# Kernel optimization log

Hardware: AMD Instinct MI355X
Metric: run time of the kernel (lower is better)

## Reference

```python
import jax, jax.numpy as jnp
import numpy as np

N_NODES = 50000
N_EDGES = 800000
D_IN = 128
D_HID = 128
GN_EPS = 1e-5
L2_EPS = 1e-12


def _gcn_conv(x, edge_index, W, b, num_nodes):
    """PyG GCNConv: symmetric normalization with self-loops; x [N, Fin]."""
    src, dst = edge_index[0], edge_index[1]
    loops = jnp.arange(num_nodes, dtype=src.dtype)
    src = jnp.concatenate([src, loops])
    dst = jnp.concatenate([dst, loops])
    ew = jnp.ones(src.shape[0], dtype=x.dtype)
    deg = jax.ops.segment_sum(ew, dst, num_segments=num_nodes)
    dinv = jnp.where(deg > 0, jax.lax.rsqrt(deg), 0.0)
    norm = dinv[src] * dinv[dst]                       # [E+N]
    xw = x @ W                                         # [N, Fout]
    msg = xw[src] * norm[:, None]                      # gather + scale
    out = jax.ops.segment_sum(msg, dst, num_segments=num_nodes)
    return out + b


def _message_norm(x, msg, scale):
    """PyG MessageNorm(learn_scale=True): x + scale * ||x|| * msg/||msg||."""
    msg_n = msg / jnp.maximum(jnp.linalg.norm(msg, axis=-1, keepdims=True), L2_EPS)
    x_norm = jnp.linalg.norm(x, axis=-1, keepdims=True)
    return x + scale * x_norm * msg_n


def _graph_norm(x, weight, bias, mean_scale):
    """PyG GraphNorm, single graph (batch all zeros)."""
    mean = jnp.mean(x, axis=0, keepdims=True)
    out = x - mean * mean_scale
    var = jnp.mean(out * out, axis=0, keepdims=True)
    return weight * out * jax.lax.rsqrt(var + GN_EPS) + bias


def _gelu(x):
    return jax.nn.gelu(x, approximate=False)


def setup_inputs() -> dict:
    key = jax.random.key(0)
    ks = jax.random.split(key, 4)
    X = jax.random.normal(ks[0], (D_IN, N_NODES), dtype=jnp.float32)
    edge_index = jax.random.randint(ks[1], (2, N_EDGES), 0, N_NODES, dtype=jnp.int64)
    W1 = jax.random.normal(ks[2], (D_IN, D_HID), dtype=jnp.float32) * (1.0 / np.sqrt(D_IN))
    b1 = jnp.zeros((D_HID,), dtype=jnp.float32)
    scale1 = jnp.ones((1,), dtype=jnp.float32)
    W2 = jax.random.normal(ks[3], (D_HID, D_IN), dtype=jnp.float32) * (1.0 / np.sqrt(D_HID))
    b2 = jnp.zeros((D_IN,), dtype=jnp.float32)
    scale2 = jnp.ones((1,), dtype=jnp.float32)
    gn_weight = jnp.ones((D_IN,), dtype=jnp.float32)
    gn_bias = jnp.zeros((D_IN,), dtype=jnp.float32)
    gn_mean_scale = jnp.ones((D_IN,), dtype=jnp.float32)
    return {"X": X, "edge_index": edge_index, "W1": W1, "b1": b1, "scale1": scale1,
            "W2": W2, "b2": b2, "scale2": scale2, "gn_weight": gn_weight,
            "gn_bias": gn_bias, "gn_mean_scale": gn_mean_scale}


def reference(X, edge_index, W1, b1, scale1, W2, b2, scale2,
              gn_weight, gn_bias, gn_mean_scale):
    x = X.T                                            # [N, D_IN]
    n = x.shape[0]
    # GCNChain 1
    f = _gelu(_message_norm(x, _gcn_conv(x, edge_index, W1, b1, n), scale1))
    # GCNChain 2
    f = _gelu(_message_norm(f, _gcn_conv(f, edge_index, W2, b2, n), scale2))
    # residual + GraphNorm + GELU
    return _gelu(_graph_norm(f + x, gn_weight, gn_bias, gn_mean_scale))
```

## Files before the change

kernel.cpp:

```cpp
#include <hip/hip_runtime.h>
#include <math.h>

#define D 128
#define CAP 64
#define NBUCK 98
#define BSZ   512
#define CAPB  10240

typedef _Float16 h8 __attribute__((ext_vector_type(8)));
typedef float f4x __attribute__((ext_vector_type(4)));

__device__ __forceinline__ float gelu_f(float v){
    return 0.5f * v * (1.0f + erff(v * 0.70710678f));
}

__global__ void k_init(float* colsum, float* colsq, int* gcur,
                       const float* __restrict__ W1, const float* __restrict__ W2,
                       _Float16* __restrict__ wz1, _Float16* __restrict__ wz2){
    int i = blockIdx.x*blockDim.x + threadIdx.x;
    if (i < D){ colsum[i] = 0.f; colsq[i] = 0.f; }
    if (i < NBUCK) gcur[i] = 0;
    if (i < 32768){
        const float* W = (i < 16384) ? W1 : W2;
        _Float16* wz   = (i < 16384) ? wz1 : wz2;
        int u = i & 16383;
        int jj = u & 7, l = (u>>3)&63, fi = u>>9;
        int kb = fi>>3, j = fi&7;
        int k = kb*32 + (l>>4)*8 + jj;
        int c = j*16 + (l&15);
        wz[u] = (_Float16)W[k*D + c];
    }
}

__global__ __launch_bounds__(256)
void k_part(const int* __restrict__ ei, int* __restrict__ gcur,
            unsigned int* __restrict__ ebin, int E){
    __shared__ int bcnt[NBUCK], bbase[NBUCK], bcur[NBUCK];
    int t = threadIdx.x;
    int chunk = (E + gridDim.x - 1) / gridDim.x;
    int e0 = blockIdx.x*chunk, e1 = min(e0 + chunk, E);
    if (t < NBUCK){ bcnt[t] = 0; bcur[t] = 0; }
    __syncthreads();
    int sl[13], dl[13];
    #pragma unroll
    for (int k = 0; k < 13; k++){
        int e = e0 + t + k*256;
        sl[k] = -1;
        if (e < e1){
            sl[k] = __builtin_nontemporal_load(&ei[e]);
            dl[k] = __builtin_nontemporal_load(&ei[E + e]);
            atomicAdd(&bcnt[dl[k] >> 9], 1);
        }
    }
    __syncthreads();
    if (t < NBUCK) bbase[t] = atomicAdd(&gcur[t], bcnt[t]);
    __syncthreads();
    #pragma unroll
    for (int k = 0; k < 13; k++){
        if (sl[k] >= 0){
            int d = dl[k], b = d >> 9;
            int p = atomicAdd(&bcur[b], 1);
            int idx = bbase[b] + p;
            if (idx < CAPB)
                ebin[(size_t)b*CAPB + idx] = ((unsigned)(d & (BSZ-1)) << 16) | (unsigned)sl[k];
        }
    }
}

__global__ __launch_bounds__(256)
void k_fill2(const unsigned int* __restrict__ ebin, const int* __restrict__ gcur,
             int* __restrict__ cnt, unsigned short* __restrict__ csrc, int N){
    __shared__ unsigned short slab[BSZ*CAP];
    __shared__ int lcnt[BSZ];
    int b = blockIdx.x, t = threadIdx.x;
    for (int i = t; i < BSZ; i += 256) lcnt[i] = 0;
    __syncthreads();
    int cntb = gcur[b]; if (cntb > CAPB) cntb = CAPB;
    const unsigned int* bp = ebin + (size_t)b*CAPB;
    for (int e = t; e < cntb; e += 256){
        unsigned pk = __builtin_nontemporal_load(&bp[e]);
        int dl = pk >> 16;
        int p = atomicAdd(&lcnt[dl], 1);
        if (p < CAP) slab[dl*CAP + p] = (unsigned short)(pk & 0xFFFF);
    }
    __syncthreads();
    int base = b*BSZ;
    int nvalid = N - base; if (nvalid > BSZ) nvalid = BSZ; if (nvalid < 0) nvalid = 0;
    uint4* dst = (uint4*)&csrc[(size_t)base*CAP];
    const uint4* src = (const uint4*)slab;
    for (int i = t; i < nvalid*8; i += 256) dst[i] = src[i];
    for (int i = t; i < nvalid; i += 256) cnt[base + i] = lcnt[i];
}

__launch_bounds__(256)
__global__ void k_gemm_mfma(const float* __restrict__ in, const h8* __restrict__ wz,
                            const int* __restrict__ cnt, _Float16* __restrict__ outh,
                            h8* __restrict__ xt16, int N){
    __shared__ _Float16 a_lds[8192];
    int t = threadIdx.x;
    int n0 = blockIdx.x * 64;

    #pragma unroll
    for (int i = 0; i < 32; i++){
        int idx = i*256 + t;
        int k = idx >> 6, nn = idx & 63;
        int n = n0 + nn;
        float v = (n < N) ? in[(size_t)k*N + n] : 0.f;
        int kb = k>>5, ks = k&31;
        int lane = (ks>>3)*16 + (nn&15);
        int w = nn>>4;
        a_lds[((kb*4 + w)*64 + lane)*8 + (ks&7)] = (_Float16)v;
    }
    __syncthreads();

    int w = t>>6, l = t&63;
    f4x acc[8];
    #pragma unroll
    for (int j = 0; j < 8; j++) acc[j] = (f4x){0.f, 0.f, 0.f, 0.f};
    #pragma unroll
    for (int kb = 0; kb < 4; kb++){
        h8 a = *(const h8*)&a_lds[((kb*4 + w)*64 + l)*8];
        #pragma unroll
        for (int j = 0; j < 8; j++){
            h8 b = wz[(kb*8 + j)*64 + l];
            acc[j] = __builtin_amdgcn_mfma_f32_16x16x32_f16(a, b, acc[j], 0, 0, 0);
        }
    }

    int quad = l>>4, m = l&15;
    #pragma unroll
    for (int r = 0; r < 4; r++){
        int node = n0 + w*16 + quad*4 + r;
        if (node < N){
            float dv = rsqrtf((float)(cnt[node] + 1));
            #pragma unroll
            for (int j = 0; j < 8; j++)
                outh[(size_t)node*D + j*16 + m] = (_Float16)(acc[j][r] * dv);
        }
    }

    {
        int node = t>>2, kb = t&3;
        int n = n0 + node;
        if (n < N){
            #pragma unroll
            for (int q = 0; q < 4; q++){
                h8 v = *(const h8*)&a_lds[((kb*4 + (node>>4))*64 + q*16 + (node&15))*8];
                xt16[(size_t)n*16 + kb*4 + q] = v;
            }
        }
    }
}

__launch_bounds__(256)
__global__ void k_gath1(const h8* __restrict__ y, const h8* __restrict__ resid,
                        const int* __restrict__ cnt,
                        const unsigned short* __restrict__ csrc,
                        const float* __restrict__ bias, const float* __restrict__ scale,
                        const h8* __restrict__ wz,
                        h8* __restrict__ f1out, _Float16* __restrict__ y2out, int N){
    __shared__ _Float16 a_lds[16*17*8];
    int t = threadIdx.x;
    int n0 = blockIdx.x * 16;
    int g = t >> 4, lane = t & 15;
    int n = n0 + g;
    bool valid = (n < N);

    h8 a0 = {0,0,0,0,0,0,0,0}, a1 = a0, a2 = a0, a3 = a0;
    int m = 0; float dv = 1.f;
    if (valid){
        int mraw = cnt[n];
        dv = rsqrtf((float)(mraw + 1));
        m = (mraw < CAP) ? mraw : CAP;
        a0 = y[(size_t)n*16 + lane];
    }
    const unsigned short* sp = csrc + (size_t)n*CAP;
    int j = 0;
    for (; j + 8 <= m; j += 8){
        int s0 = sp[j+0], s1 = sp[j+1], s2 = sp[j+2], s3 = sp[j+3];
        int s4 = sp[j+4], s5 = sp[j+5], s6 = sp[j+6], s7 = sp[j+7];
        h8 v0 = y[(size_t)s0*16 + lane];
        h8 v1 = y[(size_t)s1*16 + lane];
        h8 v2 = y[(size_t)s2*16 + lane];
        h8 v3 = y[(size_t)s3*16 + lane];
        h8 v4 = y[(size_t)s4*16 + lane];
        h8 v5 = y[(size_t)s5*16 + lane];
        h8 v6 = y[(size_t)s6*16 + lane];
        h8 v7 = y[(size_t)s7*16 + lane];
        a0 += v0; a1 += v1; a2 += v2; a3 += v3;
        a0 += v4; a1 += v5; a2 += v6; a3 += v7;
    }
    for (; j + 4 <= m; j += 4){
        int s0 = sp[j+0], s1 = sp[j+1], s2 = sp[j+2], s3 = sp[j+3];
        h8 v0 = y[(size_t)s0*16 + lane];
        h8 v1 = y[(size_t)s1*16 + lane];
        h8 v2 = y[(size_t)s2*16 + lane];
        h8 v3 = y[(size_t)s3*16 + lane];
        a0 += v0; a1 += v1; a2 += v2; a3 += v3;
    }
    for (; j < m; j++) a1 += y[(size_t)sp[j]*16 + lane];
    h8 ah = (a0 + a1) + (a2 + a3);

    const float4* bp = (const float4*)&bias[lane*8];
    float4 b0 = bp[0], b1v = bp[1];
    float c[8], r[8];
    float nc = 0.f, nr = 0.f;
    h8 rv = {0,0,0,0,0,0,0,0};
    if (valid) rv = resid[(size_t)n*16 + lane];
    #pragma unroll
    for (int i = 0; i < 8; i++){
        float bb = (i < 4) ? (&b0.x)[i] : (&b1v.x)[i-4];
        c[i] = bb + dv * (float)ah[i];
        nc += c[i]*c[i];
        r[i] = (float)rv[i];
        nr += r[i]*r[i];
    }
    #pragma unroll
    for (int mm = 8; mm > 0; mm >>= 1){
        nc += __shfl_xor(nc, mm, 64);
        nr += __shfl_xor(nr, mm, 64);
    }
    float scl = scale[0] * sqrtf(nr) / fmaxf(sqrtf(nc), 1e-12f);
    h8 o = {0,0,0,0,0,0,0,0};
    if (valid){
        #pragma unroll
        for (int i = 0; i < 8; i++) o[i] = (_Float16)gelu_f(r[i] + scl*c[i]);
        f1out[(size_t)n*16 + lane] = o;
    }
    *(h8*)&a_lds[(g*17 + lane)*8] = o;
    __syncthreads();

    int w = t >> 6, l = t & 63;
    f4x acc0 = {0.f,0.f,0.f,0.f}, acc1 = acc0;
    #pragma unroll
    for (int kb = 0; kb < 4; kb++){
        h8 a = *(const h8*)&a_lds[((l&15)*17 + kb*4 + (l>>4))*8];
        h8 bb0 = wz[(kb*8 + w*2+0)*64 + l];
        h8 bb1 = wz[(kb*8 + w*2+1)*64 + l];
        acc0 = __builtin_amdgcn_mfma_f32_16x16x32_f16(a, bb0, acc0, 0, 0, 0);
        acc1 = __builtin_amdgcn_mfma_f32_16x16x32_f16(a, bb1, acc1, 0, 0, 0);
    }
    int quad = l >> 4, mc = l & 15;
    #pragma unroll
    for (int r2 = 0; r2 < 4; r2++){
        int node = n0 + quad*4 + r2;
        if (node < N){
            float dvn = rsqrtf((float)(cnt[node] + 1));
            y2out[(size_t)node*D + (w*2+0)*16 + mc] = (_Float16)(acc0[r2] * dvn);
            y2out[(size_t)node*D + (w*2+1)*16 + mc] = (_Float16)(acc1[r2] * dvn);
        }
    }
}

__launch_bounds__(256)
__global__ void k_gather2(const h8* __restrict__ y, const h8* __restrict__ resid,
                          const h8* __restrict__ xorig,
                          const int* __restrict__ cnt,
                          const unsigned short* __restrict__ csrc,
                          const float* __restrict__ bias, const float* __restrict__ scale,
                          h8* __restrict__ out16, int N){
    int n = blockIdx.x*16 + (threadIdx.x >> 4);
    if (n >= N) return;
    int lane = threadIdx.x & 15;
    h8 a0 = y[(size_t)n*16 + lane];
    h8 a1 = {0,0,0,0,0,0,0,0}, a2 = a1, a3 = a1;
    int mraw = cnt[n];
    float dv = rsqrtf((float)(mraw + 1));
    int m = (mraw < CAP) ? mraw : CAP;
    const unsigned short* sp = csrc + (size_t)n*CAP;
    int j = 0;
    for (; j + 8 <= m; j += 8){
        int s0 = sp[j+0], s1 = sp[j+1], s2 = sp[j+2], s3 = sp[j+3];
        int s4 = sp[j+4], s5 = sp[j+5], s6 = sp[j+6], s7 = sp[j+7];
        h8 v0 = y[(size_t)s0*16 + lane];
        h8 v1 = y[(size_t)s1*16 + lane];
        h8 v2 = y[(size_t)s2*16 + lane];
        h8 v3 = y[(size_t)s3*16 + lane];
        h8 v4 = y[(size_t)s4*16 + lane];
        h8 v5 = y[(size_t)s5*16 + lane];
        h8 v6 = y[(size_t)s6*16 + lane];
        h8 v7 = y[(size_t)s7*16 + lane];
        a0 += v0; a1 += v1; a2 += v2; a3 += v3;
        a0 += v4; a1 += v5; a2 += v6; a3 += v7;
    }
    for (; j + 4 <= m; j += 4){
        int s0 = sp[j+0], s1 = sp[j+1], s2 = sp[j+2], s3 = sp[j+3];
        h8 v0 = y[(size_t)s0*16 + lane];
        h8 v1 = y[(size_t)s1*16 + lane];
        h8 v2 = y[(size_t)s2*16 + lane];
        h8 v3 = y[(size_t)s3*16 + lane];
        a0 += v0; a1 += v1; a2 += v2; a3 += v3;
    }
    for (; j < m; j++) a1 += y[(size_t)sp[j]*16 + lane];
    h8 ah = (a0 + a1) + (a2 + a3);

    const float4* bp = (const float4*)&bias[lane*8];
    float4 b0 = bp[0], b1v = bp[1];
    float c[8], r[8];
    float nc = 0.f, nr = 0.f;
    h8 rv = resid[(size_t)n*16 + lane];
    #pragma unroll
    for (int i = 0; i < 8; i++){
        float bb = (i < 4) ? (&b0.x)[i] : (&b1v.x)[i-4];
        c[i] = bb + dv * (float)ah[i];
        nc += c[i]*c[i];
        r[i] = (float)rv[i];
        nr += r[i]*r[i];
    }
    #pragma unroll
    for (int mm = 8; mm > 0; mm >>= 1){
        nc += __shfl_xor(nc, mm, 64);
        nr += __shfl_xor(nr, mm, 64);
    }
    float scl = scale[0] * sqrtf(nr) / fmaxf(sqrtf(nc), 1e-12f);
    h8 xv = xorig[(size_t)n*16 + lane];
    h8 o;
    #pragma unroll
    for (int i = 0; i < 8; i++)
        o[i] = (_Float16)(gelu_f(r[i] + scl*c[i]) + (float)xv[i]);
    out16[(size_t)n*16 + lane] = o;
}

__global__ void k_stats(const _Float16* __restrict__ h, float* colsum, float* colsq, int N){
    __shared__ float ls[256], ls2[256];
    int t = threadIdx.x;
    int f = t & 127, half = t >> 7;
    float s = 0.f, s2 = 0.f;
    for (int n = blockIdx.x*2 + half; n < N; n += gridDim.x*2){
        float v = (float)h[(size_t)n*D + f]; s += v; s2 += v*v;
    }
    ls[t] = s; ls2[t] = s2;
    __syncthreads();
    if (t < 128){
        s  = ls[t]  + ls[t+128];
        s2 = ls2[t] + ls2[t+128];
        atomicAdd(&colsum[f], s);
        atomicAdd(&colsq[f], s2);
    }
}

__global__ void k_final(const h8* __restrict__ h16,
                        const float* __restrict__ colsum, const float* __restrict__ colsq,
                        const float* __restrict__ gw, const float* __restrict__ gb,
                        const float* __restrict__ ms,
                        float* __restrict__ outp, int N){
    __shared__ float cf[D], sh[D];
    int t = threadIdx.x;
    if (t < D){
        float invN = 1.0f / (float)N;
        float mean = colsum[t] * invN;
        float c = mean * ms[t];
        float var = colsq[t]*invN - 2.f*c*mean + c*c;
        float a = gw[t] * rsqrtf(var + 1e-5f);
        cf[t] = a;
        sh[t] = gb[t] - c*a;
    }
    __syncthreads();
    int i = blockIdx.x*blockDim.x + t;
    if (i < N*16){
        int n = i >> 4, lane = i & 15;
        h8 v = h16[i];
        int f = lane*8;
        float4 o0, o1;
        o0.x = gelu_f((float)v[0]*cf[f+0] + sh[f+0]);
        o0.y = gelu_f((float)v[1]*cf[f+1] + sh[f+1]);
        o0.z = gelu_f((float)v[2]*cf[f+2] + sh[f+2]);
        o0.w = gelu_f((float)v[3]*cf[f+3] + sh[f+3]);
        o1.x = gelu_f((float)v[4]*cf[f+4] + sh[f+4]);
        o1.y = gelu_f((float)v[5]*cf[f+5] + sh[f+5]);
        o1.z = gelu_f((float)v[6]*cf[f+6] + sh[f+6]);
        o1.w = gelu_f((float)v[7]*cf[f+7] + sh[f+7]);
        *(float4*)&outp[(size_t)n*D + f]     = o0;
        *(float4*)&outp[(size_t)n*D + f + 4] = o1;
    }
}

extern "C" void kernel_launch(void* const* d_in, const int* in_sizes, int n_in,
                              void* d_out, int out_size, void* d_ws, size_t ws_size,
                              hipStream_t stream){
    const float* X   = (const float*)d_in[0];
    const int*   ei  = (const int*)  d_in[1];
    const float* W1  = (const float*)d_in[2];
    const float* b1  = (const float*)d_in[3];
    const float* s1  = (const float*)d_in[4];
    const float* W2  = (const float*)d_in[5];
    const float* b2  = (const float*)d_in[6];
    const float* s2  = (const float*)d_in[7];
    const float* gw  = (const float*)d_in[8];
    const float* gb  = (const float*)d_in[9];
    const float* gms = (const float*)d_in[10];
    int N = in_sizes[0] / D;
    int E = in_sizes[1] / 2;
    float* out = (float*)d_out;

    char* ws = (char*)d_ws;
    size_t o = 0;
    auto alloc = [&](size_t bytes)->void*{
        o = (o + 255) & ~(size_t)255;
        void* p = ws + o; o += bytes; return p;
    };
    int*            cnt    = (int*)           alloc((size_t)N * sizeof(int));
    unsigned short* csrc   = (unsigned short*)alloc((size_t)N * CAP * sizeof(unsigned short));
    unsigned int*   ebin   = (unsigned int*)  alloc((size_t)NBUCK * CAPB * sizeof(unsigned int));
    int*            gcur   = (int*)           alloc(NBUCK * sizeof(int));
    float*          colsum = (float*)         alloc(D * sizeof(float));
    float*          colsq  = (float*)         alloc(D * sizeof(float));
    _Float16*       wz1    = (_Float16*)      alloc(16384 * sizeof(_Float16));
    _Float16*       wz2    = (_Float16*)      alloc(16384 * sizeof(_Float16));
    _Float16*       A      = (_Float16*)      alloc((size_t)N * D * sizeof(_Float16));
    _Float16*       A2     = (_Float16*)      alloc((size_t)N * D * sizeof(_Float16));
    h8*             XT16   = (h8*)            alloc((size_t)N * D * sizeof(_Float16));
    h8*             F1     = (h8*)            alloc((size_t)N * D * sizeof(_Float16));
    h8*             B16    = (h8*)            alloc((size_t)N * D * sizeof(_Float16));

    k_init<<<128, 256, 0, stream>>>(colsum, colsq, gcur, W1, W2, wz1, wz2);
    k_part<<<256, 256, 0, stream>>>(ei, gcur, ebin, E);
    k_fill2<<<NBUCK, 256, 0, stream>>>(ebin, gcur, cnt, csrc, N);

    k_gemm_mfma<<<(N+63)/64, 256, 0, stream>>>(X, (const h8*)wz1, cnt, A, XT16, N);
    k_gath1<<<(N+15)/16, 256, 0, stream>>>((const h8*)A, XT16, cnt, csrc, b1, s1,
                                           (const h8*)wz2, F1, A2, N);
    k_gather2<<<(N+15)/16, 256, 0, stream>>>((const h8*)A2, F1, XT16,
                                             cnt, csrc, b2, s2, B16, N);
    k_stats<<<256, 256, 0, stream>>>((const _Float16*)B16, colsum, colsq, N);
    k_final<<<(N*16+255)/256, 256, 0, stream>>>(B16, colsum, colsq, gw, gb, gms, out, N);
}
```

Baseline: 257.8 us.

## Split gather kernels into feature-chunked aggregation and separate normalize/GELU pass

```diff
diff --git a/kernel.cpp b/kernel.cpp
--- a/kernel.cpp
+++ b/kernel.cpp
@@ -15,11 +15,13 @@
 }
 
 __global__ void k_init(float* colsum, float* colsq, int* gcur,
+                       float* nc1, float* nr1, float* nc2, float* nr2,
                        const float* __restrict__ W1, const float* __restrict__ W2,
-                       _Float16* __restrict__ wz1, _Float16* __restrict__ wz2){
+                       _Float16* __restrict__ wz1, _Float16* __restrict__ wz2, int N){
     int i = blockIdx.x*blockDim.x + threadIdx.x;
     if (i < D){ colsum[i] = 0.f; colsq[i] = 0.f; }
     if (i < NBUCK) gcur[i] = 0;
+    if (i < N){ nc1[i] = 0.f; nr1[i] = 0.f; nc2[i] = 0.f; nr2[i] = 0.f; }
     if (i < 32768){
         const float* W = (i < 16384) ? W1 : W2;
         _Float16* wz   = (i < 16384) ? wz1 : wz2;
@@ -153,78 +155,96 @@
 }
 
 __launch_bounds__(256)
-__global__ void k_gath1(const h8* __restrict__ y, const h8* __restrict__ resid,
-                        const int* __restrict__ cnt,
-                        const unsigned short* __restrict__ csrc,
-                        const float* __restrict__ bias, const float* __restrict__ scale,
-                        const h8* __restrict__ wz,
-                        h8* __restrict__ f1out, _Float16* __restrict__ y2out, int N){
-    __shared__ _Float16 a_lds[16*17*8];
-    int t = threadIdx.x;
-    int n0 = blockIdx.x * 16;
-    int g = t >> 4, lane = t & 15;
+__global__ void k_gA(const h8* __restrict__ y, const h8* __restrict__ resid,
+                     const int* __restrict__ cnt, const unsigned short* __restrict__ csrc,
+                     const float* __restrict__ bias,
+                     h8* __restrict__ cbuf, float* __restrict__ ncArr,
+                     float* __restrict__ nrArr, int N){
+    int t = threadIdx.x;
+    int fc = blockIdx.x & 3;
+    int n0 = (blockIdx.x >> 2) * 64;
+    int g = t >> 2, l4 = t & 3;
     int n = n0 + g;
-    bool valid = (n < N);
-
-    h8 a0 = {0,0,0,0,0,0,0,0}, a1 = a0, a2 = a0, a3 = a0;
-    int m = 0; float dv = 1.f;
-    if (valid){
-        int mraw = cnt[n];
-        dv = rsqrtf((float)(mraw + 1));
-        m = (mraw < CAP) ? mraw : CAP;
-        a0 = y[(size_t)n*16 + lane];
-    }
+    if (n >= N) return;
+    int ci = fc*4 + l4;
+
+    int mraw = cnt[n];
+    float dv = rsqrtf((float)(mraw + 1));
+    int m = (mraw < CAP) ? mraw : CAP;
+    h8 a0 = y[(size_t)n*16 + ci];
+    h8 a1 = {0,0,0,0,0,0,0,0}, a2 = a1, a3 = a1;
     const unsigned short* sp = csrc + (size_t)n*CAP;
     int j = 0;
     for (; j + 8 <= m; j += 8){
         int s0 = sp[j+0], s1 = sp[j+1], s2 = sp[j+2], s3 = sp[j+3];
         int s4 = sp[j+4], s5 = sp[j+5], s6 = sp[j+6], s7 = sp[j+7];
-        h8 v0 = y[(size_t)s0*16 + lane];
-        h8 v1 = y[(size_t)s1*16 + lane];
-        h8 v2 = y[(size_t)s2*16 + lane];
-        h8 v3 = y[(size_t)s3*16 + lane];
-        h8 v4 = y[(size_t)s4*16 + lane];
-        h8 v5 = y[(size_t)s5*16 + lane];
-        h8 v6 = y[(size_t)s6*16 + lane];
-        h8 v7 = y[(size_t)s7*16 + lane];
+        h8 v0 = y[(size_t)s0*16 + ci];
+        h8 v1 = y[(size_t)s1*16 + ci];
+        h8 v2 = y[(size_t)s2*16 + ci];
+        h8 v3 = y[(size_t)s3*16 + ci];
+        h8 v4 = y[(size_t)s4*16 + ci];
+        h8 v5 = y[(size_t)s5*16 + ci];
+        h8 v6 = y[(size_t)s6*16 + ci];
+        h8 v7 = y[(size_t)s7*16 + ci];
         a0 += v0; a1 += v1; a2 += v2; a3 += v3;
         a0 += v4; a1 += v5; a2 += v6; a3 += v7;
     }
     for (; j + 4 <= m; j += 4){
         int s0 = sp[j+0], s1 = sp[j+1], s2 = sp[j+2], s3 = sp[j+3];
-        h8 v0 = y[(size_t)s0*16 + lane];
-        h8 v1 = y[(size_t)s1*16 + lane];
-        h8 v2 = y[(size_t)s2*16 + lane];
-        h8 v3 = y[(size_t)s3*16 + lane];
+        h8 v0 = y[(size_t)s0*16 + ci];
+        h8 v1 = y[(size_t)s1*16 + ci];
+        h8 v2 = y[(size_t)s2*16 + ci];
+        h8 v3 = y[(size_t)s3*16 + ci];
         a0 += v0; a1 += v1; a2 += v2; a3 += v3;
     }
-    for (; j < m; j++) a1 += y[(size_t)sp[j]*16 + lane];
+    for (; j < m; j++) a1 += y[(size_t)sp[j]*16 + ci];
     h8 ah = (a0 + a1) + (a2 + a3);
 
-    const float4* bp = (const float4*)&bias[lane*8];
+    const float4* bp = (const float4*)&bias[ci*8];
     float4 b0 = bp[0], b1v = bp[1];
-    float c[8], r[8];
+    h8 rv = resid[(size_t)n*16 + ci];
     float nc = 0.f, nr = 0.f;
-    h8 rv = {0,0,0,0,0,0,0,0};
-    if (valid) rv = resid[(size_t)n*16 + lane];
+    h8 co;
     #pragma unroll
     for (int i = 0; i < 8; i++){
         float bb = (i < 4) ? (&b0.x)[i] : (&b1v.x)[i-4];
-        c[i] = bb + dv * (float)ah[i];
-        nc += c[i]*c[i];
-        r[i] = (float)rv[i];
-        nr += r[i]*r[i];
-    }
-    #pragma unroll
-    for (int mm = 8; mm > 0; mm >>= 1){
-        nc += __shfl_xor(nc, mm, 64);
-        nr += __shfl_xor(nr, mm, 64);
-    }
-    float scl = scale[0] * sqrtf(nr) / fmaxf(sqrtf(nc), 1e-12f);
+        float c = bb + dv * (float)ah[i];
+        nc += c*c;
+        float r = (float)rv[i];
+        nr += r*r;
+        co[i] = (_Float16)c;
+    }
+    cbuf[(size_t)n*16 + ci] = co;
+    nc += __shfl_xor(nc, 1, 64); nc += __shfl_xor(nc, 2, 64);
+    nr += __shfl_xor(nr, 1, 64); nr += __shfl_xor(nr, 2, 64);
+    if (l4 == 0){
+        atomicAdd(&ncArr[n], nc);
+        atomicAdd(&nrArr[n], nr);
+    }
+}
+
+__launch_bounds__(256)
+__global__ void k_gB1(const h8* __restrict__ cbuf, const h8* __restrict__ resid,
+                      const float* __restrict__ ncArr, const float* __restrict__ nrArr,
+                      const float* __restrict__ scale, const int* __restrict__ cnt,
+                      const h8* __restrict__ wz,
+                      h8* __restrict__ f1out, _Float16* __restrict__ y2out, int N){
+    __shared__ _Float16 a_lds[16*17*8];
+    int t = threadIdx.x;
+    int n0 = blockIdx.x * 16;
+    int g = t >> 4, lane = t & 15;
+    int n = n0 + g;
+    bool valid = (n < N);
+
     h8 o = {0,0,0,0,0,0,0,0};
     if (valid){
+        float nc = ncArr[n], nr = nrArr[n];
+        float scl = scale[0] * sqrtf(nr) / fmaxf(sqrtf(nc), 1e-12f);
+        h8 cv = cbuf[(size_t)n*16 + lane];
+        h8 rv = resid[(size_t)n*16 + lane];
         #pragma unroll
-        for (int i = 0; i < 8; i++) o[i] = (_Float16)gelu_f(r[i] + scl*c[i]);
+        for (int i = 0; i < 8; i++)
+            o[i] = (_Float16)gelu_f((float)rv[i] + scl*(float)cv[i]);
         f1out[(size_t)n*16 + lane] = o;
     }
     *(h8*)&a_lds[(g*17 + lane)*8] = o;
@@ -253,71 +273,23 @@
 }
 
 __launch_bounds__(256)
-__global__ void k_gather2(const h8* __restrict__ y, const h8* __restrict__ resid,
-                          const h8* __restrict__ xorig,
-                          const int* __restrict__ cnt,
-                          const unsigned short* __restrict__ csrc,
-                          const float* __restrict__ bias, const float* __restrict__ scale,
-                          h8* __restrict__ out16, int N){
-    int n = blockIdx.x*16 + (threadIdx.x >> 4);
-    if (n >= N) return;
-    int lane = threadIdx.x & 15;
-    h8 a0 = y[(size_t)n*16 + lane];
-    h8 a1 = {0,0,0,0,0,0,0,0}, a2 = a1, a3 = a1;
-    int mraw = cnt[n];
-    float dv = rsqrtf((float)(mraw + 1));
-    int m = (mraw < CAP) ? mraw : CAP;
-    const unsigned short* sp = csrc + (size_t)n*CAP;
-    int j = 0;
-    for (; j + 8 <= m; j += 8){
-        int s0 = sp[j+0], s1 = sp[j+1], s2 = sp[j+2], s3 = sp[j+3];
-        int s4 = sp[j+4], s5 = sp[j+5], s6 = sp[j+6], s7 = sp[j+7];
-        h8 v0 = y[(size_t)s0*16 + lane];
-        h8 v1 = y[(size_t)s1*16 + lane];
-        h8 v2 = y[(size_t)s2*16 + lane];
-        h8 v3 = y[(size_t)s3*16 + lane];
-        h8 v4 = y[(size_t)s4*16 + lane];
-        h8 v5 = y[(size_t)s5*16 + lane];
-        h8 v6 = y[(size_t)s6*16 + lane];
-        h8 v7 = y[(size_t)s7*16 + lane];
-        a0 += v0; a1 += v1; a2 += v2; a3 += v3;
-        a0 += v4; a1 += v5; a2 += v6; a3 += v7;
-    }
-    for (; j + 4 <= m; j += 4){
-        int s0 = sp[j+0], s1 = sp[j+1], s2 = sp[j+2], s3 = sp[j+3];
-        h8 v0 = y[(size_t)s0*16 + lane];
-        h8 v1 = y[(size_t)s1*16 + lane];
-        h8 v2 = y[(size_t)s2*16 + lane];
-        h8 v3 = y[(size_t)s3*16 + lane];
-        a0 += v0; a1 += v1; a2 += v2; a3 += v3;
-    }
-    for (; j < m; j++) a1 += y[(size_t)sp[j]*16 + lane];
-    h8 ah = (a0 + a1) + (a2 + a3);
-
-    const float4* bp = (const float4*)&bias[lane*8];
-    float4 b0 = bp[0], b1v = bp[1];
-    float c[8], r[8];
-    float nc = 0.f, nr = 0.f;
+__global__ void k_gB2(const h8* __restrict__ cbuf, const h8* __restrict__ resid,
+                      const h8* __restrict__ xorig,
+                      const float* __restrict__ ncArr, const float* __restrict__ nrArr,
+                      const float* __restrict__ scale,
+                      h8* __restrict__ out16, int N){
+    int i = blockIdx.x*blockDim.x + threadIdx.x;
+    if (i >= N*16) return;
+    int n = i >> 4, lane = i & 15;
+    float nc = ncArr[n], nr = nrArr[n];
+    float scl = scale[0] * sqrtf(nr) / fmaxf(sqrtf(nc), 1e-12f);
+    h8 cv = cbuf[(size_t)n*16 + lane];
     h8 rv = resid[(size_t)n*16 + lane];
-    #pragma unroll
-    for (int i = 0; i < 8; i++){
-        float bb = (i < 4) ? (&b0.x)[i] : (&b1v.x)[i-4];
-        c[i] = bb + dv * (float)ah[i];
-        nc += c[i]*c[i];
-        r[i] = (float)rv[i];
-        nr += r[i]*r[i];
-    }
-    #pragma unroll
-    for (int mm = 8; mm > 0; mm >>= 1){
-        nc += __shfl_xor(nc, mm, 64);
-        nr += __shfl_xor(nr, mm, 64);
-    }
-    float scl = scale[0] * sqrtf(nr) / fmaxf(sqrtf(nc), 1e-12f);
     h8 xv = xorig[(size_t)n*16 + lane];
     h8 o;
     #pragma unroll
-    for (int i = 0; i < 8; i++)
-        o[i] = (_Float16)(gelu_f(r[i] + scl*c[i]) + (float)xv[i]);
+    for (int k = 0; k < 8; k++)
+        o[k] = (_Float16)(gelu_f((float)rv[k] + scl*(float)cv[k]) + (float)xv[k]);
     out16[(size_t)n*16 + lane] = o;
 }
 
@@ -405,23 +377,33 @@
     int*            gcur   = (int*)           alloc(NBUCK * sizeof(int));
     float*          colsum = (float*)         alloc(D * sizeof(float));
     float*          colsq  = (float*)         alloc(D * sizeof(float));
+    float*          nc1    = (float*)         alloc((size_t)N * sizeof(float));
+    float*          nr1    = (float*)         alloc((size_t)N * sizeof(float));
+    float*          nc2    = (float*)         alloc((size_t)N * sizeof(float));
+    float*          nr2    = (float*)         alloc((size_t)N * sizeof(float));
     _Float16*       wz1    = (_Float16*)      alloc(16384 * sizeof(_Float16));
     _Float16*       wz2    = (_Float16*)      alloc(16384 * sizeof(_Float16));
     _Float16*       A      = (_Float16*)      alloc((size_t)N * D * sizeof(_Float16));
     _Float16*       A2     = (_Float16*)      alloc((size_t)N * D * sizeof(_Float16));
     h8*             XT16   = (h8*)            alloc((size_t)N * D * sizeof(_Float16));
     h8*             F1     = (h8*)            alloc((size_t)N * D * sizeof(_Float16));
+    h8*             C1     = (h8*)            alloc((size_t)N * D * sizeof(_Float16));
+    h8*             C2     = (h8*)            alloc((size_t)N * D * sizeof(_Float16));
     h8*             B16    = (h8*)            alloc((size_t)N * D * sizeof(_Float16));
 
-    k_init<<<128, 256, 0, stream>>>(colsum, colsq, gcur, W1, W2, wz1, wz2);
+    k_init<<<(N+255)/256, 256, 0, stream>>>(colsum, colsq, gcur, nc1, nr1, nc2, nr2,
+                                            W1, W2, wz1, wz2, N);
     k_part<<<256, 256, 0, stream>>>(ei, gcur, ebin, E);
     k_fill2<<<NBUCK, 256, 0, stream>>>(ebin, gcur, cnt, csrc, N);
 
     k_gemm_mfma<<<(N+63)/64, 256, 0, stream>>>(X, (const h8*)wz1, cnt, A, XT16, N);
-    k_gath1<<<(N+15)/16, 256, 0, stream>>>((const h8*)A, XT16, cnt, csrc, b1, s1,
-                                           (const h8*)wz2, F1, A2, N);
-    k_gather2<<<(N+15)/16, 256, 0, stream>>>((const h8*)A2, F1, XT16,
-                                             cnt, csrc, b2, s2, B16, N);
+    k_gA<<<4*((N+63)/64), 256, 0, stream>>>((const h8*)A, XT16, cnt, csrc, b1,
+                                            C1, nc1, nr1, N);
+    k_gB1<<<(N+15)/16, 256, 0, stream>>>(C1, XT16, nc1, nr1, s1, cnt,
+                                         (const h8*)wz2, F1, A2, N);
+    k_gA<<<4*((N+63)/64), 256, 0, stream>>>((const h8*)A2, F1, cnt, csrc, b2,
+                                            C2, nc2, nr2, N);
+    k_gB2<<<(N*16+255)/256, 256, 0, stream>>>(C2, F1, XT16, nc2, nr2, s2, B16, N);
     k_stats<<<256, 256, 0, stream>>>((const _Float16*)B16, colsum, colsq, N);
     k_final<<<(N*16+255)/256, 256, 0, stream>>>(B16, colsum, colsq, gw, gb, gms, out, N);
 }
```

Result: slower. 312.7 us (+21.3%).
